# Performance work log

Hardware: AMD Instinct MI355X
Metric: run time of the kernel (lower is better)

## Reference

```python
import jax, jax.numpy as jnp
import numpy as np

NET_DIM = 512
INPUT_DIM = 1024
DEPTH = 2
HEADS = 8
DIM_HEAD = NET_DIM // HEADS  # 64
MLP_DIM = NET_DIM * 4        # 2048
SCALE = DIM_HEAD ** -0.5


def layer_norm(x, g, b, eps=1e-5):
    mu = jnp.mean(x, axis=-1, keepdims=True)
    var = jnp.var(x, axis=-1, keepdims=True)
    return (x - mu) * jax.lax.rsqrt(var + eps) * g + b


def sinusoidal_pos_emb(klen, demb):
    # pos_seq = [klen-1, ..., 0]; emb = [sin(pos*inv_freq), cos(pos*inv_freq)]
    pos_seq = jnp.arange(klen - 1, -1, -1, dtype=jnp.float32)
    inv_freq = 1.0 / (10000.0 ** (jnp.arange(0, demb, 2, dtype=jnp.float32) / demb))
    sinusoid = pos_seq[:, None] * inv_freq[None, :]  # [klen, demb/2]
    return jnp.concatenate([jnp.sin(sinusoid), jnp.cos(sinusoid)], axis=-1)  # [klen, demb]


def setup_inputs() -> dict:
    key = jax.random.key(0)
    ks = jax.random.split(key, 16)
    B, N = 2, 4096
    mem_len = 8
    s = 0.02
    inp = {
        'data': jax.random.normal(ks[0], (B, N, INPUT_DIM), jnp.float32),
        'mems': jax.random.normal(ks[1], (DEPTH, B, mem_len, NET_DIM), jnp.float32),
        'fc1_w': jax.random.normal(ks[2], (INPUT_DIM, NET_DIM), jnp.float32) * s,
        'fc1_b': jnp.zeros((NET_DIM,), jnp.float32),
        'cls_token': jax.random.normal(ks[3], (1, 1, NET_DIM), jnp.float32),
        'ln1_g': jnp.ones((DEPTH, NET_DIM), jnp.float32),
        'ln1_b': jnp.zeros((DEPTH, NET_DIM), jnp.float32),
        'qkv_w': jax.random.normal(ks[4], (DEPTH, NET_DIM, 3 * NET_DIM), jnp.float32) * s,
        'out_w': jax.random.normal(ks[5], (DEPTH, NET_DIM, NET_DIM), jnp.float32) * s,
        'out_b': jnp.zeros((DEPTH, NET_DIM), jnp.float32),
        'ln2_g': jnp.ones((DEPTH, NET_DIM), jnp.float32),
        'ln2_b': jnp.zeros((DEPTH, NET_DIM), jnp.float32),
        'ff_w1': jax.random.normal(ks[6], (DEPTH, NET_DIM, MLP_DIM), jnp.float32) * s,
        'ff_b1': jnp.zeros((DEPTH, MLP_DIM), jnp.float32),
        'ff_w2': jax.random.normal(ks[7], (DEPTH, MLP_DIM, NET_DIM), jnp.float32) * s,
        'ff_b2': jnp.zeros((DEPTH, NET_DIM), jnp.float32),
        'normf_g': jnp.ones((NET_DIM,), jnp.float32),
        'normf_b': jnp.zeros((NET_DIM,), jnp.float32),
        'fc2_w': jax.random.normal(ks[8], (NET_DIM, 2), jnp.float32) * s,
        'fc2_b': jnp.zeros((2,), jnp.float32),
    }
    return inp


def reference(data, mems, fc1_w, fc1_b, cls_token,
              ln1_g, ln1_b, qkv_w, out_w, out_b,
              ln2_g, ln2_b, ff_w1, ff_b1, ff_w2, ff_b2,
              normf_g, normf_b, fc2_w, fc2_b):
    B = data.shape[0]
    # fc1 + ReLU
    h = jax.nn.relu(jnp.einsum('bnf,fd->bnd', data, fc1_w) + fc1_b)  # [B, N, 512]
    # prepend cls token
    x = jnp.concatenate([jnp.broadcast_to(cls_token, (B, 1, NET_DIM)), h], axis=1)  # [B, N+1, 512]
    n = x.shape[1]
    mem_len = mems.shape[2]
    klen = n + mem_len
    pos_emb = sinusoidal_pos_emb(klen, NET_DIM)  # [klen, 512]

    for i in range(DEPTH):
        # attention with memory concat + additive sinusoidal pos-emb on k/v
        xa = layer_norm(x, ln1_g[i], ln1_b[i])
        qkv = jnp.einsum('bnd,de->bne', xa, qkv_w[i])  # [B, n, 1536]
        q, k, v = jnp.split(qkv, 3, axis=-1)
        k = jnp.concatenate([k, mems[i]], axis=1) + pos_emb  # [B, klen, 512]
        v = jnp.concatenate([v, mems[i]], axis=1) + pos_emb
        q = q.reshape(B, n, HEADS, DIM_HEAD).transpose(0, 2, 1, 3)      # [B, h, n, d]
        k = k.reshape(B, klen, HEADS, DIM_HEAD).transpose(0, 2, 1, 3)   # [B, h, klen, d]
        v = v.reshape(B, klen, HEADS, DIM_HEAD).transpose(0, 2, 1, 3)
        dots = jnp.einsum('bhnd,bhkd->bhnk', q, k) * SCALE
        attn = jax.nn.softmax(dots, axis=-1)
        out = jnp.einsum('bhnk,bhkd->bhnd', attn, v)
        out = out.transpose(0, 2, 1, 3).reshape(B, n, NET_DIM)
        out = jnp.einsum('bnd,de->bne', out, out_w[i]) + out_b[i]
        x = x + out
        # feed-forward (pre-LN, exact GELU)
        xf = layer_norm(x, ln2_g[i], ln2_b[i])
        xf = jax.nn.gelu(jnp.einsum('bnd,dh->bnh', xf, ff_w1[i]) + ff_b1[i], approximate=False)
        xf = jnp.einsum('bnh,hd->bnd', xf, ff_w2[i]) + ff_b2[i]
        x = x + xf

    x = layer_norm(x, normf_g, normf_b)
    logits = x[:, 0] @ fc2_w + fc2_b  # [B, n_classes]
    return logits
```

## Files before the change

kernel.cpp:

```cpp
#include <hip/hip_runtime.h>
#include <hip/hip_bf16.h>
#include <math.h>

#define B_SZ   2
#define NTOK   4097
#define KLEN   4105
#define KLEN_PAD 4160
#define DMODEL 512
#define INDIM  1024
#define NHEAD  8
#define DHEAD  64
#define MLPD   2048
#define MEMLEN 8
#define NEG_BIG  -1.0e30f
#define CSCALE 0.18033688f
#define NQT 65
#define SPLIT_MID 33
#define NSPLIT1 17
#define CH1 256

typedef unsigned short ushort_t;
typedef short bf16x8 __attribute__((ext_vector_type(8)));
typedef float f32x4  __attribute__((ext_vector_type(4)));

__device__ __forceinline__ unsigned short f2bf(float f) {
    union { float f; unsigned u; } v; v.f = f;
    const unsigned r = v.u + 0x7fff + ((v.u >> 16) & 1);
    return (unsigned short)(r >> 16);
}
__device__ __forceinline__ unsigned short f2bf_rhu(float f) {
    union { float f; unsigned u; } v; v.f = f;
    return (unsigned short)((v.u + 0x8000u) >> 16);
}
__device__ __forceinline__ float bf2f(unsigned short u) {
    union { unsigned u; float f; } v; v.u = ((unsigned)u) << 16;
    return v.f;
}

__device__ __forceinline__ void gload_lds16(const void* g, void* l) {
    __builtin_amdgcn_global_load_lds(
        (const __attribute__((address_space(1))) unsigned int*)g,
        (__attribute__((address_space(3))) unsigned int*)l, 16, 0, 0);
}

__device__ __forceinline__ float block_reduce_sum_256(float v, float* sh) {
    #pragma unroll
    for (int m = 1; m < 64; m <<= 1) v += __shfl_xor(v, m);
    const int w = threadIdx.x >> 6;
    if ((threadIdx.x & 63) == 0) sh[w] = v;
    __syncthreads();
    float r = sh[0] + sh[1] + sh[2] + sh[3];
    __syncthreads();
    return r;
}

__global__ void k_pos(float* __restrict__ pos) {
    const int p = blockIdx.x;
    const int j = threadIdx.x;
    const float position = (float)(KLEN - 1 - p);
    const float inv_freq = exp2f(-(float)j * 0.051905126f);
    const float x = position * inv_freq;
    pos[(long)p * DMODEL + j]       = __sinf(x);
    pos[(long)p * DMODEL + 256 + j] = __cosf(x);
}

__global__ void k_cls(const float* __restrict__ cls, float* __restrict__ x) {
    const int b = blockIdx.x;
    x[(long)b * NTOK * DMODEL + threadIdx.x] = cls[threadIdx.x];
}

__global__ __launch_bounds__(256)
void k_f2b(const float* __restrict__ in, ushort_t* __restrict__ out, long n4) {
    for (long i = blockIdx.x * 256 + threadIdx.x; i < n4; i += (long)gridDim.x * 256) {
        const float4 f = ((const float4*)in)[i];
        ushort4 u;
        u.x = f2bf(f.x); u.y = f2bf(f.y); u.z = f2bf(f.z); u.w = f2bf(f.w);
        ((ushort4*)out)[i] = u;
    }
}

__global__ __launch_bounds__(256)
void k_w2bt(const float* __restrict__ W, ushort_t* __restrict__ Wt, int K, int N) {
    __shared__ float tile[64][65];
    W  += (long)blockIdx.z * K * N;
    Wt += (long)blockIdx.z * N * K;
    const int n0 = blockIdx.x * 64, k0 = blockIdx.y * 64;
    const int t = threadIdx.x;
    #pragma unroll
    for (int rep = 0; rep < 16; ++rep) {
        const int idx = rep * 256 + t;
        const int r = idx >> 6, c = idx & 63;
        tile[r][c] = W[(long)(k0 + r) * N + n0 + c];
    }
    __syncthreads();
    #pragma unroll
    for (int rep = 0; rep < 16; ++rep) {
        const int idx = rep * 256 + t;
        const int n = idx >> 6, kk = idx & 63;
        Wt[(long)(n0 + n) * K + k0 + kk] = f2bf(tile[kk][n]);
    }
}

enum { EPI_NONE = 0, EPI_BIAS_RELU = 1, EPI_BIAS_GELU = 2, EPI_BIAS_RES = 3 };

template <int EPI, int OBF16>
__global__ __launch_bounds__(256)
void k_gemm_bf(const ushort_t* __restrict__ A, const ushort_t* __restrict__ Wt,
               const float* __restrict__ bias, void* __restrict__ Cv,
               int M, int K, int N, long ldc, long sAb, long sCb)
{
    __shared__ ushort_t As[128 * 64];
    __shared__ ushort_t Bs[128 * 64];
    const int t    = threadIdx.x;
    const int lane = t & 63;
    const int w    = t >> 6;
    const int l15  = lane & 15;
    const int lhi  = lane >> 4;
    const int wr   = w >> 1, wc = w & 1;
    const long bm = (long)blockIdx.y * 128, bn = (long)blockIdx.x * 128;
    A += (long)blockIdx.z * sAb;
    float*    Cf = (float*)Cv    + (long)blockIdx.z * sCb;
    ushort_t* Cb = (ushort_t*)Cv + (long)blockIdx.z * sCb;

    int srow[4], scol[4];
    #pragma unroll
    for (int i = 0; i < 4; ++i) {
        const int c = i * 256 + t;
        srow[i] = c >> 3;
        scol[i] = ((c & 7) ^ (srow[i] & 7)) << 3;
    }

    f32x4 acc[4][4] = {};

    for (int k0 = 0; k0 < K; k0 += 64) {
        __syncthreads();
        #pragma unroll
        for (int i = 0; i < 4; ++i) {
            long ar = bm + srow[i]; if (ar >= M) ar = M - 1;
            gload_lds16(A + ar * (long)K + k0 + scol[i],
                        &As[(i * 256 + (t & ~63)) * 8]);
        }
        #pragma unroll
        for (int i = 0; i < 4; ++i) {
            gload_lds16(Wt + (bn + srow[i]) * (long)K + k0 + scol[i],
                        &Bs[(i * 256 + (t & ~63)) * 8]);
        }
        asm volatile("s_waitcnt vmcnt(0)" ::: "memory");
        __syncthreads();

        #pragma unroll
        for (int ks = 0; ks < 2; ++ks) {
            bf16x8 af[4], bfr[4];
            #pragma unroll
            for (int m = 0; m < 4; ++m) {
                const int row = wr * 64 + m * 16 + l15;
                const int cb  = (ks * 64 + lhi * 16) ^ ((row & 7) << 4);
                af[m] = *(const bf16x8*)((const char*)As + row * 128 + cb);
            }
            #pragma unroll
            for (int n = 0; n < 4; ++n) {
                const int row = wc * 64 + n * 16 + l15;
                const int cb  = (ks * 64 + lhi * 16) ^ ((row & 7) << 4);
                bfr[n] = *(const bf16x8*)((const char*)Bs + row * 128 + cb);
            }
            #pragma unroll
            for (int m = 0; m < 4; ++m)
                #pragma unroll
                for (int n = 0; n < 4; ++n)
                    acc[m][n] = __builtin_amdgcn_mfma_f32_16x16x32_bf16(af[m], bfr[n], acc[m][n], 0, 0, 0);
        }
    }

    #pragma unroll
    for (int m = 0; m < 4; ++m) {
        #pragma unroll
        for (int j = 0; j < 4; ++j) {
            const long mg = bm + wr * 64 + m * 16 + lhi * 4 + j;
            if (mg < M) {
                #pragma unroll
                for (int n = 0; n < 4; ++n) {
                    const long ng = bn + wc * 64 + n * 16 + l15;
                    float r = acc[m][n][j];
                    if (EPI != EPI_NONE) r += bias[ng];
                    if (EPI == EPI_BIAS_RELU) r = fmaxf(r, 0.f);
                    if (EPI == EPI_BIAS_GELU) r = 0.5f * r * (1.f + erff(r * 0.70710678118654752f));
                    if (OBF16) Cb[mg * ldc + ng] = f2bf(r);
                    else if (EPI == EPI_BIAS_RES) Cf[mg * ldc + ng] += r;
                    else Cf[mg * ldc + ng] = r;
                }
            }
        }
    }
}

template <int EPI, int OBF16>
__global__ __launch_bounds__(256)
void k_gemv(const ushort_t* __restrict__ A, const ushort_t* __restrict__ Wt,
            const float* __restrict__ bias, void* __restrict__ Cv,
            int K, int N, long sA, long sC)
{
    const int b = blockIdx.y;
    const int n = blockIdx.x * 64 + (threadIdx.x >> 2);
    const int j = threadIdx.x & 3;
    const ushort_t* a = A + (long)b * sA;
    const ushort_t* wv = Wt + (long)n * K;
    float sum = 0.f;
    for (int k0 = j * 8; k0 < K; k0 += 32) {
        const bf16x8 av = *(const bf16x8*)(a + k0);
        const bf16x8 wr = *(const bf16x8*)(wv + k0);
        #pragma unroll
        for (int e = 0; e < 8; ++e)
            sum += bf2f((ushort_t)av[e]) * bf2f((ushort_t)wr[e]);
    }
    sum += __shfl_xor(sum, 1);
    sum += __shfl_xor(sum, 2);
    if (j == 0 && n < N) {
        float r = sum;
        if (EPI != EPI_NONE) r += bias[n];
        if (EPI == EPI_BIAS_GELU) r = 0.5f * r * (1.f + erff(r * 0.70710678118654752f));
        if (OBF16) ((ushort_t*)Cv)[(long)b * sC + n] = f2bf(r);
        else if (EPI == EPI_BIAS_RES) ((float*)Cv)[(long)b * sC + n] += r;
        else ((float*)Cv)[(long)b * sC + n] = r;
    }
}

__global__ __launch_bounds__(256)
void k_ln(const float* __restrict__ x, ushort_t* __restrict__ y,
          const float* __restrict__ g, const float* __restrict__ b, long rstride)
{
    __shared__ float sh[4];
    const long row = (long)blockIdx.x * rstride;
    const float* xr = x + row * DMODEL;
    const int t = threadIdx.x;
    const float v0 = xr[t], v1 = xr[t + 256];
    const float s  = block_reduce_sum_256(v0 + v1, sh);
    const float s2 = block_reduce_sum_256(v0 * v0 + v1 * v1, sh);
    const float mu = s * (1.f / DMODEL);
    const float var = s2 * (1.f / DMODEL) - mu * mu;
    const float rs = rsqrtf(var + 1e-5f);
    y[row * DMODEL + t]       = f2bf((v0 - mu) * rs * g[t] + b[t]);
    y[row * DMODEL + t + 256] = f2bf((v1 - mu) * rs * g[t + 256] + b[t + 256]);
}

__global__ __launch_bounds__(256)
void k_build_k(const ushort_t* __restrict__ qkvb, const float* __restrict__ mems,
               const float* __restrict__ pos, ushort_t* __restrict__ kf, int layer)
{
    const int b = blockIdx.y;
    const long idx = (long)blockIdx.x * 256 + threadIdx.x;
    const int j  = (int)(idx >> 7);
    const int d0 = (int)(idx & 127) * 4;
    if (j >= KLEN) return;
    float v0, v1, v2, v3;
    if (j < NTOK) {
        const ushort_t* s = qkvb + ((long)b * NTOK + j) * 1536 + 512 + d0;
        v0 = bf2f(s[0]); v1 = bf2f(s[1]); v2 = bf2f(s[2]); v3 = bf2f(s[3]);
    } else {
        const float* mb = mems + (((long)layer * B_SZ + b) * MEMLEN + (j - NTOK)) * DMODEL + d0;
        v0 = mb[0]; v1 = mb[1]; v2 = mb[2]; v3 = mb[3];
    }
    const float4 pe = *(const float4*)(pos + (long)j * DMODEL + d0);
    ushort4 o;
    o.x = f2bf((v0 + pe.x) * CSCALE);
    o.y = f2bf((v1 + pe.y) * CSCALE);
    o.z = f2bf((v2 + pe.z) * CSCALE);
    o.w = f2bf((v3 + pe.w) * CSCALE);
    *(ushort4*)(kf + ((long)b * KLEN + j) * DMODEL + d0) = o;
}

__global__ __launch_bounds__(256)
void k_build_vt(const ushort_t* __restrict__ qkvb, const float* __restrict__ mems,
                const float* __restrict__ pos, ushort_t* __restrict__ vt, int layer)
{
    __shared__ ushort_t tile[64][65];
    const int jb = blockIdx.x * 64;
    const int b  = blockIdx.y;
    const int h  = blockIdx.z;
    const int t  = threadIdx.x;
    #pragma unroll
    for (int rep = 0; rep < 16; ++rep) {
        const int idx = rep * 256 + t;
        const int r = idx >> 6, c = idx & 63;
        const int j = jb + r;
        float val = 0.f;
        if (j < NTOK)
            val = bf2f(qkvb[((long)b * NTOK + j) * 1536 + 1024 + h * 64 + c]) + pos[(long)j * DMODEL + h * 64 + c];
        else if (j < KLEN)
            val = mems[(((long)layer * B_SZ + b) * MEMLEN + (j - NTOK)) * DMODEL + h * 64 + c]
                + pos[(long)j * DMODEL + h * 64 + c];
        tile[c][r] = f2bf(val);
    }
    __syncthreads();
    #pragma unroll
    for (int rep = 0; rep < 16; ++rep) {
        const int idx = rep * 256 + t;
        const int d = idx >> 6, r = idx & 63;
        vt[(((long)b * NHEAD + h) * 64 + d) * (long)KLEN_PAD + jb + r] = tile[d][r];
    }
}

#define LDSP 72

__global__ __launch_bounds__(256)
void k_attn_sp(const ushort_t* __restrict__ qkvb,
               const ushort_t* __restrict__ kf,
               const ushort_t* __restrict__ vt,
               ushort_t* __restrict__ part0,
               ushort_t* __restrict__ part1,
               float2* __restrict__ ml)
{
    __shared__ ushort_t QPs[64][LDSP];
    __shared__ ushort_t Ks [64][LDSP];
    __shared__ ushort_t Vts[64][LDSP];

    const int t     = threadIdx.x;
    const int lane  = t & 63;
    const int w     = t >> 6;
    const int l15   = lane & 15;
    const int lhi   = lane >> 4;
    const int qt    = blockIdx.x;
    const int qb    = qt * 64;
    const int split = blockIdx.y >> 3;
    const int h     = blockIdx.y & 7;
    const int b     = blockIdx.z;
    const int ktBeg = split ? SPLIT_MID : 0;
    const int ktEnd = split ? NQT : SPLIT_MID;
    ushort_t* part  = split ? part1 : part0;

    {
        const int r  = t >> 2;
        const int c0 = (t & 3) * 16;
        const int qg = qb + r;
        uint4 u0 = make_uint4(0,0,0,0), u1 = make_uint4(0,0,0,0);
        if (qg < NTOK) {
            const ushort_t* src = qkvb + ((long)b * NTOK + qg) * 1536 + h * 64 + c0;
            u0 = ((const uint4*)src)[0];
            u1 = ((const uint4*)src)[1];
        }
        *(uint4*)&QPs[r][c0]     = u0;
        *(uint4*)&QPs[r][c0 + 8] = u1;
    }
    __syncthreads();
    bf16x8 q_frag[2];
    #pragma unroll
    for (int ks = 0; ks < 2; ++ks)
        q_frag[ks] = *(const bf16x8*)&QPs[w * 16 + l15][ks * 32 + lhi * 8];

    f32x4 o_frag[4] = {};
    float m_run[4] = {NEG_BIG, NEG_BIG, NEG_BIG, NEG_BIG};
    float l_run[4] = {0.f, 0.f, 0.f, 0.f};

    const ushort_t* kbase = kf + (long)b * KLEN * DMODEL + h * 64;
    const ushort_t* vbase = vt + ((long)b * NHEAD + h) * 64 * (long)KLEN_PAD;

    for (int kt = ktBeg; kt < ktEnd; ++kt) {
        const int kb = kt * 64;
        __syncthreads();
        {
            const int r = t >> 2;
            const int jg = kb + r;
            #pragma unroll
            for (int cc = 0; cc < 2; ++cc) {
                const int c8 = (t & 3) * 2 + cc;
                uint4 kv = make_uint4(0u, 0u, 0u, 0u);
                if (jg < KLEN) kv = *(const uint4*)(kbase + (long)jg * DMODEL + c8 * 8);
                *(uint4*)&Ks[r][c8 * 8] = kv;
                const uint4 vv = *(const uint4*)(vbase + (long)r * KLEN_PAD + kb + c8 * 8);
                *(uint4*)&Vts[r][c8 * 8] = vv;
            }
        }
        __syncthreads();

        f32x4 s_frag[4];
        #pragma unroll
        for (int n = 0; n < 4; ++n) {
            f32x4 acc = {0.f, 0.f, 0.f, 0.f};
            #pragma unroll
            for (int ks = 0; ks < 2; ++ks) {
                const bf16x8 kfr = *(const bf16x8*)&Ks[n * 16 + l15][ks * 32 + lhi * 8];
                acc = __builtin_amdgcn_mfma_f32_16x16x32_bf16(q_frag[ks], kfr, acc, 0, 0, 0);
            }
            s_frag[n] = acc;
        }

        #pragma unroll
        for (int i = 0; i < 4; ++i) {
            float sv[4];
            #pragma unroll
            for (int n = 0; n < 4; ++n) sv[n] = s_frag[n][i];
            if (kt == NQT - 1) {
                #pragma unroll
                for (int n = 0; n < 4; ++n)
                    if (kb + n * 16 + l15 >= KLEN) sv[n] = NEG_BIG;
            }
            float mx = fmaxf(fmaxf(sv[0], sv[1]), fmaxf(sv[2], sv[3]));
            mx = fmaxf(mx, __shfl_xor(mx, 1));
            mx = fmaxf(mx, __shfl_xor(mx, 2));
            mx = fmaxf(mx, __shfl_xor(mx, 4));
            mx = fmaxf(mx, __shfl_xor(mx, 8));
            const float mnew  = fmaxf(m_run[i], mx);
            const float alpha = exp2f(m_run[i] - mnew);
            float lsum = 0.f;
            ushort_t pb[4];
            #pragma unroll
            for (int n = 0; n < 4; ++n) {
                const float p = exp2f(sv[n] - mnew);
                lsum += p;
                pb[n] = f2bf_rhu(p);
            }
            lsum += __shfl_xor(lsum, 1);
            lsum += __shfl_xor(lsum, 2);
            lsum += __shfl_xor(lsum, 4);
            lsum += __shfl_xor(lsum, 8);
            l_run[i] = l_run[i] * alpha + lsum;
            m_run[i] = mnew;
            #pragma unroll
            for (int n = 0; n < 4; ++n) {
                o_frag[n][i] *= alpha;
                QPs[w * 16 + lhi * 4 + i][n * 16 + l15] = pb[n];
            }
        }
        __syncthreads();

        #pragma unroll
        for (int n = 0; n < 4; ++n) {
            #pragma unroll
            for (int ks = 0; ks < 2; ++ks) {
                const bf16x8 pa = *(const bf16x8*)&QPs[w * 16 + l15][ks * 32 + lhi * 8];
                const bf16x8 vb = *(const bf16x8*)&Vts[n * 16 + l15][ks * 32 + lhi * 8];
                o_frag[n] = __builtin_amdgcn_mfma_f32_16x16x32_bf16(pa, vb, o_frag[n], 0, 0, 0);
            }
        }
    }

    #pragma unroll
    for (int i = 0; i < 4; ++i) {
        const int r  = w * 16 + lhi * 4 + i;
        const int rg = qb + r;
        if (rg < NTOK) {
            ushort_t* op = part + ((long)b * NTOK + rg) * DMODEL + h * 64 + l15;
            #pragma unroll
            for (int n = 0; n < 4; ++n) op[n * 16] = f2bf(o_frag[n][i]);
            if (l15 == 0)
                ml[(((long)split * B_SZ + b) * NHEAD + h) * (NQT * 64) + (long)qt * 64 + r]
                    = make_float2(m_run[i], l_run[i]);
        }
    }
}

__global__ __launch_bounds__(256)
void k_comb(ushort_t* __restrict__ part0, const ushort_t* __restrict__ part1,
            const float2* __restrict__ ml)
{
    const int qt = blockIdx.x, h = blockIdx.y, b = blockIdx.z;
    const int t  = threadIdx.x;
    const int r  = t >> 2;
    const int c0 = (t & 3) * 16;
    const int rg = qt * 64 + r;
    if (rg >= NTOK) return;
    const long mli = ((long)b * NHEAD + h) * (NQT * 64) + (long)qt * 64 + r;
    const float2 a0 = ml[mli];
    const float2 a1 = ml[(long)B_SZ * NHEAD * NQT * 64 + mli];
    const float M  = fmaxf(a0.x, a1.x);
    const float e0 = exp2f(a0.x - M);
    const float e1 = exp2f(a1.x - M);
    const float inv = 1.f / (a0.y * e0 + a1.y * e1);
    ushort_t*       p0 = part0 + ((long)b * NTOK + rg) * DMODEL + h * 64 + c0;
    const ushort_t* p1 = part1 + ((long)b * NTOK + rg) * DMODEL + h * 64 + c0;
    #pragma unroll
    for (int c = 0; c < 16; ++c)
        p0[c] = f2bf((bf2f(p0[c]) * e0 + bf2f(p1[c]) * e1) * inv);
}

__global__ __launch_bounds__(256)
void k_attn1_sp(const ushort_t* __restrict__ qkvb, const float* __restrict__ mems,
                const float* __restrict__ pos, float* __restrict__ part)
{
    __shared__ float qs[64];
    __shared__ float sarr[CH1];
    __shared__ float red[4];
    __shared__ float osum[4][64];
    const int sp = blockIdx.x, h = blockIdx.y, b = blockIdx.z;
    const int t = threadIdx.x, w = t >> 6;
    const int j0 = sp * CH1;
    const int jend = min(j0 + CH1, KLEN);

    if (t < 64) qs[t] = bf2f(qkvb[(long)b * NTOK * 1536 + h * 64 + t]);
    __syncthreads();

    const int j = j0 + t;
    float s = NEG_BIG;
    if (j < KLEN) {
        float acc = 0.f;
        const float* pp = pos + (long)j * DMODEL + h * 64;
        if (j < NTOK) {
            const ushort_t* kr = qkvb + ((long)b * NTOK + j) * 1536 + 512 + h * 64;
            #pragma unroll
            for (int d = 0; d < 64; ++d) acc += qs[d] * (bf2f(kr[d]) + pp[d]);
        } else {
            const float* mb = mems + (((long)B_SZ + b) * MEMLEN + (j - NTOK)) * DMODEL + h * 64;
            #pragma unroll
            for (int d = 0; d < 64; ++d) acc += qs[d] * (mb[d] + pp[d]);
        }
        s = acc * CSCALE;
    }
    float mx = s;
    #pragma unroll
    for (int m = 1; m < 64; m <<= 1) mx = fmaxf(mx, __shfl_xor(mx, m));
    if ((t & 63) == 0) red[w] = mx;
    __syncthreads();
    const float M = fmaxf(fmaxf(red[0], red[1]), fmaxf(red[2], red[3]));
    __syncthreads();

    const float p = (j < KLEN) ? exp2f(s - M) : 0.f;
    sarr[t] = p;
    float lsum = p;
    #pragma unroll
    for (int m = 1; m < 64; m <<= 1) lsum += __shfl_xor(lsum, m);
    if ((t & 63) == 0) red[w] = lsum;
    __syncthreads();
    const float L = red[0] + red[1] + red[2] + red[3];

    const int d = t & 63, g = t >> 6;
    float o = 0.f;
    for (int j2 = j0 + g; j2 < jend; j2 += 4) {
        float v;
        if (j2 < NTOK) v = bf2f(qkvb[((long)b * NTOK + j2) * 1536 + 1024 + h * 64 + d]);
        else           v = mems[(((long)B_SZ + b) * MEMLEN + (j2 - NTOK)) * DMODEL + h * 64 + d];
        v += pos[(long)j2 * DMODEL + h * 64 + d];
        o += sarr[j2 - j0] * v;
    }
    osum[g][d] = o;
    __syncthreads();
    if (t < 64) {
        float* pb = part + (((long)b * NHEAD + h) * NSPLIT1 + sp) * 66;
        pb[2 + t] = osum[0][t] + osum[1][t] + osum[2][t] + osum[3][t];
        if (t == 0) { pb[0] = M; pb[1] = L; }
    }
}

__global__ __launch_bounds__(64)
void k_attn1_cb(const float* __restrict__ part, ushort_t* __restrict__ outp)
{
    const int h = blockIdx.x, b = blockIdx.y;
    const int t = threadIdx.x;
    const float* pb = part + ((long)b * NHEAD + h) * NSPLIT1 * 66;
    float M = NEG_BIG;
    #pragma unroll
    for (int c = 0; c < NSPLIT1; ++c) M = fmaxf(M, pb[c * 66]);
    float L = 0.f, o = 0.f;
    #pragma unroll
    for (int c = 0; c < NSPLIT1; ++c) {
        const float e = exp2f(pb[c * 66] - M);
        L += e * pb[c * 66 + 1];
        o += e * pb[c * 66 + 2 + t];
    }
    outp[(long)b * NTOK * DMODEL + h * 64 + t] = f2bf(o / L);
}

__global__ __launch_bounds__(256)
void k_final(const float* __restrict__ x, const float* __restrict__ g,
             const float* __restrict__ bb, const float* __restrict__ w2,
             const float* __restrict__ b2, float* __restrict__ out)
{
    __shared__ float sh[4];
    const int b = blockIdx.x;
    const float* xr = x + (long)b * NTOK * DMODEL;
    const int t = threadIdx.x;
    const float v0 = xr[t], v1 = xr[t + 256];
    const float s  = block_reduce_sum_256(v0 + v1, sh);
    const float s2 = block_reduce_sum_256(v0 * v0 + v1 * v1, sh);
    const float mu = s * (1.f / DMODEL);
    const float var = s2 * (1.f / DMODEL) - mu * mu;
    const float rs = rsqrtf(var + 1e-5f);
    const float n0 = (v0 - mu) * rs * g[t] + bb[t];
    const float n1 = (v1 - mu) * rs * g[t + 256] + bb[t + 256];
    const float p0 = block_reduce_sum_256(n0 * w2[t * 2 + 0] + n1 * w2[(t + 256) * 2 + 0], sh);
    const float p1 = block_reduce_sum_256(n0 * w2[t * 2 + 1] + n1 * w2[(t + 256) * 2 + 1], sh);
    if (t == 0) {
        out[b * 2 + 0] = p0 + b2[0];
        out[b * 2 + 1] = p1 + b2[1];
    }
}

extern "C" void kernel_launch(void* const* d_in, const int* in_sizes, int n_in,
                              void* d_out, int out_size, void* d_ws, size_t ws_size,
                              hipStream_t stream)
{
    const float* data    = (const float*)d_in[0];
    const float* mems    = (const float*)d_in[1];
    const float* fc1_w   = (const float*)d_in[2];
    const float* fc1_b   = (const float*)d_in[3];
    const float* cls     = (const float*)d_in[4];
    const float* ln1_g   = (const float*)d_in[5];
    const float* ln1_b   = (const float*)d_in[6];
    const float* qkv_w   = (const float*)d_in[7];
    const float* out_w   = (const float*)d_in[8];
    const float* out_b   = (const float*)d_in[9];
    const float* ln2_g   = (const float*)d_in[10];
    const float* ln2_b   = (const float*)d_in[11];
    const float* ff_w1   = (const float*)d_in[12];
    const float* ff_b1   = (const float*)d_in[13];
    const float* ff_w2   = (const float*)d_in[14];
    const float* ff_b2   = (const float*)d_in[15];
    const float* normf_g = (const float*)d_in[16];
    const float* normf_b = (const float*)d_in[17];
    const float* fc2_w   = (const float*)d_in[18];
    const float* fc2_b   = (const float*)d_in[19];
    float* out = (float*)d_out;

    const int MROWS = B_SZ * NTOK;
    const int MT128 = (MROWS + 127) / 128;
    const long XROW = (long)NTOK * DMODEL;

    char* p = (char*)d_ws;
    float* x   = (float*)p;            p += (long)B_SZ * NTOK * DMODEL * 4;
    float* pos = (float*)p;            p += (long)KLEN * DMODEL * 4;
    ushort_t* data_bf = (ushort_t*)p;  p += (long)B_SZ * 4096 * INDIM * 2;
    ushort_t* actA    = (ushort_t*)p;  p += (long)MROWS * DMODEL * 2;
    ushort_t* actB    = (ushort_t*)p;  p += (long)MROWS * DMODEL * 2;
    ushort_t* fc1_wt  = (ushort_t*)p;  p += (long)DMODEL * INDIM * 2;
    ushort_t* qkv_wt  = (ushort_t*)p;  p += (long)2 * 1536 * DMODEL * 2;
    ushort_t* out_wt  = (ushort_t*)p;  p += (long)2 * DMODEL * DMODEL * 2;
    ushort_t* ff1_wt  = (ushort_t*)p;  p += (long)2 * MLPD * DMODEL * 2;
    ushort_t* ff2_wt  = (ushort_t*)p;  p += (long)2 * DMODEL * MLPD * 2;
    ushort_t* qkv_bf  = (ushort_t*)p;
    ushort_t* kf      = qkv_bf + (long)MROWS * 1536;
    ushort_t* vt      = kf + (long)B_SZ * KLEN * DMODEL;
    ushort_t* ffbuf   = qkv_bf;

    ushort_t* part1 = data_bf;
    float2*   mlbuf = (float2*)(data_bf + (long)B_SZ * NTOK * DMODEL);
    float*    dec_part = (float*)(mlbuf + (long)2 * B_SZ * NHEAD * NQT * 64);

    k_f2b<<<dim3(2048), dim3(256), 0, stream>>>(data, data_bf, (long)B_SZ * 4096 * INDIM / 4);
    k_w2bt<<<dim3(DMODEL/64, INDIM/64, 1),  dim3(256), 0, stream>>>(fc1_w, fc1_wt, INDIM, DMODEL);
    k_w2bt<<<dim3(1536/64, DMODEL/64, 2),   dim3(256), 0, stream>>>(qkv_w, qkv_wt, DMODEL, 1536);
    k_w2bt<<<dim3(DMODEL/64, DMODEL/64, 2), dim3(256), 0, stream>>>(out_w, out_wt, DMODEL, DMODEL);
    k_w2bt<<<dim3(MLPD/64, DMODEL/64, 2),   dim3(256), 0, stream>>>(ff_w1, ff1_wt, DMODEL, MLPD);
    k_w2bt<<<dim3(DMODEL/64, MLPD/64, 2),   dim3(256), 0, stream>>>(ff_w2, ff2_wt, MLPD, DMODEL);

    k_pos<<<dim3(KLEN), dim3(256), 0, stream>>>(pos);
    k_cls<<<dim3(B_SZ), dim3(512), 0, stream>>>(cls, x);

    k_gemm_bf<EPI_BIAS_RELU, 0><<<dim3(DMODEL/128, 4096/128, B_SZ), dim3(256), 0, stream>>>(
        data_bf, fc1_wt, fc1_b, x + DMODEL, 4096, INDIM, DMODEL, DMODEL,
        (long)4096 * INDIM, XROW);

    const int KBK = (KLEN * 128 + 255) / 256;

    {
        k_ln<<<dim3(MROWS), dim3(256), 0, stream>>>(x, actA, ln1_g, ln1_b, 1);
        k_gemm_bf<EPI_NONE, 1><<<dim3(1536/128, MT128, 1), dim3(256), 0, stream>>>(
            actA, qkv_wt, nullptr, qkv_bf, MROWS, DMODEL, 1536, 1536, 0, 0);
        k_build_k <<<dim3(KBK, B_SZ), dim3(256), 0, stream>>>(qkv_bf, mems, pos, kf, 0);
        k_build_vt<<<dim3(KLEN_PAD/64, B_SZ, NHEAD), dim3(256), 0, stream>>>(qkv_bf, mems, pos, vt, 0);
        k_attn_sp<<<dim3(NQT, 16, B_SZ), dim3(256), 0, stream>>>(qkv_bf, kf, vt, actB, part1, mlbuf);
        k_comb   <<<dim3(NQT, NHEAD, B_SZ), dim3(256), 0, stream>>>(actB, part1, mlbuf);
        k_gemm_bf<EPI_BIAS_RES, 0><<<dim3(DMODEL/128, MT128, 1), dim3(256), 0, stream>>>(
            actB, out_wt, out_b, x, MROWS, DMODEL, DMODEL, DMODEL, 0, 0);
        k_ln<<<dim3(MROWS), dim3(256), 0, stream>>>(x, actA, ln2_g, ln2_b, 1);
        k_gemm_bf<EPI_BIAS_GELU, 1><<<dim3(MLPD/128, MT128, 1), dim3(256), 0, stream>>>(
            actA, ff1_wt, ff_b1, ffbuf, MROWS, DMODEL, MLPD, MLPD, 0, 0);
        k_gemm_bf<EPI_BIAS_RES, 0><<<dim3(DMODEL/128, MT128, 1), dim3(256), 0, stream>>>(
            ffbuf, ff2_wt, ff_b2, x, MROWS, MLPD, DMODEL, DMODEL, 0, 0);
    }

    {
        k_ln<<<dim3(MROWS), dim3(256), 0, stream>>>(x, actA, ln1_g + DMODEL, ln1_b + DMODEL, 1);
        k_gemm_bf<EPI_NONE, 1><<<dim3(1024/128, MT128, 1), dim3(256), 0, stream>>>(
            actA, qkv_wt + (long)1536 * DMODEL + (long)512 * DMODEL, nullptr, qkv_bf + 512,
            MROWS, DMODEL, 1024, 1536, 0, 0);
        k_gemv<EPI_NONE, 1><<<dim3(512/64, B_SZ), dim3(256), 0, stream>>>(
            actA, qkv_wt + (long)1536 * DMODEL, nullptr, qkv_bf,
            DMODEL, 512, (long)NTOK * DMODEL, (long)NTOK * 1536);
        k_attn1_sp<<<dim3(NSPLIT1, NHEAD, B_SZ), dim3(256), 0, stream>>>(qkv_bf, mems, pos, dec_part);
        k_attn1_cb<<<dim3(NHEAD, B_SZ), dim3(64), 0, stream>>>(dec_part, actB);
        k_gemv<EPI_BIAS_RES, 0><<<dim3(512/64, B_SZ), dim3(256), 0, stream>>>(
            actB, out_wt + (long)DMODEL * DMODEL, out_b + DMODEL, x,
            DMODEL, 512, (long)NTOK * DMODEL, XROW);
        k_ln<<<dim3(B_SZ), dim3(256), 0, stream>>>(x, actA, ln2_g + DMODEL, ln2_b + DMODEL, NTOK);
        k_gemv<EPI_BIAS_GELU, 1><<<dim3(MLPD/64, B_SZ), dim3(256), 0, stream>>>(
            actA, ff1_wt + (long)MLPD * DMODEL, ff_b1 + MLPD, ffbuf,
            DMODEL, MLPD, (long)NTOK * DMODEL, MLPD);
        k_gemv<EPI_BIAS_RES, 0><<<dim3(512/64, B_SZ), dim3(256), 0, stream>>>(
            ffbuf, ff2_wt + (long)DMODEL * MLPD, ff_b2 + DMODEL, x,
            MLPD, 512, MLPD, XROW);
    }

    k_final<<<dim3(B_SZ), dim3(256), 0, stream>>>(x, normf_g, normf_b, fc2_w, fc2_b, out);
}
```

Baseline: 746.5 us.

## Add 64x64 GEMM tile for narrow outputs and defer softmax rescaling in attention

Adds a 64x64-tile bf16 MFMA GEMM kernel and uses it for the fc1, out-projection and FF2 GEMMs, whose 512-wide outputs gave too few 128x128 blocks to fill the GPU. In the split attention kernel, the QK MFMA operands are swapped so each lane holds one query row. This turns the row max/sum reductions into two cross-lane shuffles, and the running max is updated lazily only when a new max exceeds it by a threshold, skipping most alpha rescales. The risks are reduced per-block data reuse in the smaller GEMM and a larger bounded exponent range under the deferred max. The diff also drops a __syncthreads after P is written to shared memory, which could race if lanes read other lanes' P rows.

```diff
diff --git a/kernel.cpp b/kernel.cpp
--- a/kernel.cpp
+++ b/kernel.cpp
@@ -18,6 +18,7 @@
 #define SPLIT_MID 33
 #define NSPLIT1 17
 #define CH1 256
+#define DEFER_THR 8.0f
 
 typedef unsigned short ushort_t;
 typedef short bf16x8 __attribute__((ext_vector_type(8)));
@@ -195,6 +196,84 @@
 
 template <int EPI, int OBF16>
 __global__ __launch_bounds__(256)
+void k_gemm_bf64(const ushort_t* __restrict__ A, const ushort_t* __restrict__ Wt,
+                 const float* __restrict__ bias, void* __restrict__ Cv,
+                 int M, int K, int N, long ldc, long sAb, long sCb)
+{
+    __shared__ ushort_t As[64 * 64];
+    __shared__ ushort_t Bs[64 * 64];
+    const int t    = threadIdx.x;
+    const int lane = t & 63;
+    const int w    = t >> 6;
+    const int l15  = lane & 15;
+    const int lhi  = lane >> 4;
+    const long bm = (long)blockIdx.y * 64, bn = (long)blockIdx.x * 64;
+    A += (long)blockIdx.z * sAb;
+    float*    Cf = (float*)Cv    + (long)blockIdx.z * sCb;
+    ushort_t* Cb = (ushort_t*)Cv + (long)blockIdx.z * sCb;
+
+    int srow[2], scol[2];
+    #pragma unroll
+    for (int i = 0; i < 2; ++i) {
+        const int c = i * 256 + t;
+        srow[i] = c >> 3;
+        scol[i] = ((c & 7) ^ (srow[i] & 7)) << 3;
+    }
+
+    f32x4 acc[4] = {};
+
+    for (int k0 = 0; k0 < K; k0 += 64) {
+        __syncthreads();
+        #pragma unroll
+        for (int i = 0; i < 2; ++i) {
+            long ar = bm + srow[i]; if (ar >= M) ar = M - 1;
+            gload_lds16(A + ar * (long)K + k0 + scol[i],
+                        &As[(i * 256 + (t & ~63)) * 8]);
+        }
+        #pragma unroll
+        for (int i = 0; i < 2; ++i) {
+            gload_lds16(Wt + (bn + srow[i]) * (long)K + k0 + scol[i],
+                        &Bs[(i * 256 + (t & ~63)) * 8]);
+        }
+        asm volatile("s_waitcnt vmcnt(0)" ::: "memory");
+        __syncthreads();
+
+        #pragma unroll
+        for (int ks = 0; ks < 2; ++ks) {
+            const int rowa = w * 16 + l15;
+            const int cba  = (ks * 64 + lhi * 16) ^ ((rowa & 7) << 4);
+            const bf16x8 af = *(const bf16x8*)((const char*)As + rowa * 128 + cba);
+            #pragma unroll
+            for (int n = 0; n < 4; ++n) {
+                const int rowb = n * 16 + l15;
+                const int cbb  = (ks * 64 + lhi * 16) ^ ((rowb & 7) << 4);
+                const bf16x8 bfr = *(const bf16x8*)((const char*)Bs + rowb * 128 + cbb);
+                acc[n] = __builtin_amdgcn_mfma_f32_16x16x32_bf16(af, bfr, acc[n], 0, 0, 0);
+            }
+        }
+    }
+
+    #pragma unroll
+    for (int j = 0; j < 4; ++j) {
+        const long mg = bm + w * 16 + lhi * 4 + j;
+        if (mg < M) {
+            #pragma unroll
+            for (int n = 0; n < 4; ++n) {
+                const long ng = bn + n * 16 + l15;
+                float r = acc[n][j];
+                if (EPI != EPI_NONE) r += bias[ng];
+                if (EPI == EPI_BIAS_RELU) r = fmaxf(r, 0.f);
+                if (EPI == EPI_BIAS_GELU) r = 0.5f * r * (1.f + erff(r * 0.70710678118654752f));
+                if (OBF16) Cb[mg * ldc + ng] = f2bf(r);
+                else if (EPI == EPI_BIAS_RES) Cf[mg * ldc + ng] += r;
+                else Cf[mg * ldc + ng] = r;
+            }
+        }
+    }
+}
+
+template <int EPI, int OBF16>
+__global__ __launch_bounds__(256)
 void k_gemv(const ushort_t* __restrict__ A, const ushort_t* __restrict__ Wt,
             const float* __restrict__ bias, void* __restrict__ Cv,
             int K, int N, long sA, long sC)
@@ -347,8 +426,8 @@
         q_frag[ks] = *(const bf16x8*)&QPs[w * 16 + l15][ks * 32 + lhi * 8];
 
     f32x4 o_frag[4] = {};
-    float m_run[4] = {NEG_BIG, NEG_BIG, NEG_BIG, NEG_BIG};
-    float l_run[4] = {0.f, 0.f, 0.f, 0.f};
+    float m_run = NEG_BIG;
+    float l_run = 0.f;
 
     const ushort_t* kbase = kf + (long)b * KLEN * DMODEL + h * 64;
     const ushort_t* vbase = vt + ((long)b * NHEAD + h) * 64 * (long)KLEN_PAD;
@@ -378,49 +457,59 @@
             #pragma unroll
             for (int ks = 0; ks < 2; ++ks) {
                 const bf16x8 kfr = *(const bf16x8*)&Ks[n * 16 + l15][ks * 32 + lhi * 8];
-                acc = __builtin_amdgcn_mfma_f32_16x16x32_bf16(q_frag[ks], kfr, acc, 0, 0, 0);
+                acc = __builtin_amdgcn_mfma_f32_16x16x32_bf16(kfr, q_frag[ks], acc, 0, 0, 0);
             }
             s_frag[n] = acc;
         }
 
-        #pragma unroll
-        for (int i = 0; i < 4; ++i) {
-            float sv[4];
-            #pragma unroll
-            for (int n = 0; n < 4; ++n) sv[n] = s_frag[n][i];
-            if (kt == NQT - 1) {
+        if (kt == NQT - 1) {
+            #pragma unroll
+            for (int n = 0; n < 4; ++n)
                 #pragma unroll
-                for (int n = 0; n < 4; ++n)
-                    if (kb + n * 16 + l15 >= KLEN) sv[n] = NEG_BIG;
-            }
-            float mx = fmaxf(fmaxf(sv[0], sv[1]), fmaxf(sv[2], sv[3]));
-            mx = fmaxf(mx, __shfl_xor(mx, 1));
-            mx = fmaxf(mx, __shfl_xor(mx, 2));
-            mx = fmaxf(mx, __shfl_xor(mx, 4));
-            mx = fmaxf(mx, __shfl_xor(mx, 8));
-            const float mnew  = fmaxf(m_run[i], mx);
-            const float alpha = exp2f(m_run[i] - mnew);
-            float lsum = 0.f;
-            ushort_t pb[4];
-            #pragma unroll
-            for (int n = 0; n < 4; ++n) {
-                const float p = exp2f(sv[n] - mnew);
-                lsum += p;
-                pb[n] = f2bf_rhu(p);
-            }
-            lsum += __shfl_xor(lsum, 1);
-            lsum += __shfl_xor(lsum, 2);
-            lsum += __shfl_xor(lsum, 4);
-            lsum += __shfl_xor(lsum, 8);
-            l_run[i] = l_run[i] * alpha + lsum;
-            m_run[i] = mnew;
-            #pragma unroll
-            for (int n = 0; n < 4; ++n) {
-                o_frag[n][i] *= alpha;
-                QPs[w * 16 + lhi * 4 + i][n * 16 + l15] = pb[n];
-            }
-        }
-        __syncthreads();
+                for (int i = 0; i < 4; ++i)
+                    if (kb + n * 16 + lhi * 4 + i >= KLEN) s_frag[n][i] = NEG_BIG;
+        }
+
+        float tmax = NEG_BIG;
+        #pragma unroll
+        for (int n = 0; n < 4; ++n)
+            #pragma unroll
+            for (int i = 0; i < 4; ++i)
+                tmax = fmaxf(tmax, s_frag[n][i]);
+        tmax = fmaxf(tmax, __shfl_xor(tmax, 16));
+        tmax = fmaxf(tmax, __shfl_xor(tmax, 32));
+
+        if (__any(tmax > m_run + DEFER_THR)) {
+            const float mnew  = fmaxf(m_run, tmax);
+            const float alpha = exp2f(m_run - mnew);
+            m_run = mnew;
+            l_run *= alpha;
+            float al[4];
+            #pragma unroll
+            for (int i = 0; i < 4; ++i) al[i] = __shfl(alpha, lhi * 4 + i);
+            #pragma unroll
+            for (int n = 0; n < 4; ++n)
+                #pragma unroll
+                for (int i = 0; i < 4; ++i)
+                    o_frag[n][i] *= al[i];
+        }
+
+        float lsum = 0.f;
+        #pragma unroll
+        for (int n = 0; n < 4; ++n) {
+            ushort4 pk;
+            float p0 = exp2f(s_frag[n][0] - m_run);
+            float p1 = exp2f(s_frag[n][1] - m_run);
+            float p2 = exp2f(s_frag[n][2] - m_run);
+            float p3 = exp2f(s_frag[n][3] - m_run);
+            lsum += (p0 + p1) + (p2 + p3);
+            pk.x = f2bf_rhu(p0); pk.y = f2bf_rhu(p1);
+            pk.z = f2bf_rhu(p2); pk.w = f2bf_rhu(p3);
+            *(ushort4*)&QPs[w * 16 + l15][n * 16 + lhi * 4] = pk;
+        }
+        lsum += __shfl_xor(lsum, 16);
+        lsum += __shfl_xor(lsum, 32);
+        l_run += lsum;
 
         #pragma unroll
         for (int n = 0; n < 4; ++n) {
@@ -435,16 +524,18 @@
 
     #pragma unroll
     for (int i = 0; i < 4; ++i) {
-        const int r  = w * 16 + lhi * 4 + i;
-        const int rg = qb + r;
+        const int rg = qb + w * 16 + lhi * 4 + i;
         if (rg < NTOK) {
             ushort_t* op = part + ((long)b * NTOK + rg) * DMODEL + h * 64 + l15;
             #pragma unroll
             for (int n = 0; n < 4; ++n) op[n * 16] = f2bf(o_frag[n][i]);
-            if (l15 == 0)
-                ml[(((long)split * B_SZ + b) * NHEAD + h) * (NQT * 64) + (long)qt * 64 + r]
-                    = make_float2(m_run[i], l_run[i]);
-        }
+        }
+    }
+    {
+        const int rg = qb + w * 16 + l15;
+        if (lhi == 0 && rg < NTOK)
+            ml[(((long)split * B_SZ + b) * NHEAD + h) * (NQT * 64) + (long)qt * 64 + w * 16 + l15]
+                = make_float2(m_run, l_run);
     }
 }
 
@@ -611,6 +702,7 @@
 
     const int MROWS = B_SZ * NTOK;
     const int MT128 = (MROWS + 127) / 128;
+    const int MT64  = (MROWS + 63) / 64;
     const long XROW = (long)NTOK * DMODEL;
 
     char* p = (char*)d_ws;
@@ -643,7 +735,7 @@
     k_pos<<<dim3(KLEN), dim3(256), 0, stream>>>(pos);
     k_cls<<<dim3(B_SZ), dim3(512), 0, stream>>>(cls, x);
 
-    k_gemm_bf<EPI_BIAS_RELU, 0><<<dim3(DMODEL/128, 4096/128, B_SZ), dim3(256), 0, stream>>>(
+    k_gemm_bf64<EPI_BIAS_RELU, 0><<<dim3(DMODEL/64, 4096/64, B_SZ), dim3(256), 0, stream>>>(
         data_bf, fc1_wt, fc1_b, x + DMODEL, 4096, INDIM, DMODEL, DMODEL,
         (long)4096 * INDIM, XROW);
 
@@ -657,12 +749,12 @@
         k_build_vt<<<dim3(KLEN_PAD/64, B_SZ, NHEAD), dim3(256), 0, stream>>>(qkv_bf, mems, pos, vt, 0);
         k_attn_sp<<<dim3(NQT, 16, B_SZ), dim3(256), 0, stream>>>(qkv_bf, kf, vt, actB, part1, mlbuf);
         k_comb   <<<dim3(NQT, NHEAD, B_SZ), dim3(256), 0, stream>>>(actB, part1, mlbuf);
-        k_gemm_bf<EPI_BIAS_RES, 0><<<dim3(DMODEL/128, MT128, 1), dim3(256), 0, stream>>>(
+        k_gemm_bf64<EPI_BIAS_RES, 0><<<dim3(DMODEL/64, MT64, 1), dim3(256), 0, stream>>>(
             actB, out_wt, out_b, x, MROWS, DMODEL, DMODEL, DMODEL, 0, 0);
         k_ln<<<dim3(MROWS), dim3(256), 0, stream>>>(x, actA, ln2_g, ln2_b, 1);
         k_gemm_bf<EPI_BIAS_GELU, 1><<<dim3(MLPD/128, MT128, 1), dim3(256), 0, stream>>>(
             actA, ff1_wt, ff_b1, ffbuf, MROWS, DMODEL, MLPD, MLPD, 0, 0);
-        k_gemm_bf<EPI_BIAS_RES, 0><<<dim3(DMODEL/128, MT128, 1), dim3(256), 0, stream>>>(
+        k_gemm_bf64<EPI_BIAS_RES, 0><<<dim3(DMODEL/64, MT64, 1), dim3(256), 0, stream>>>(
             ffbuf, ff2_wt, ff_b2, x, MROWS, MLPD, DMODEL, DMODEL, 0, 0);
     }
 
```

Measured after the change: 622.7 us. -16.6%, faster.
